# Kernel tuning notes

Measured on AMD Instinct MI355X. Metric: run time of the kernel, lower is better.

Reference implementation:

```python
import jax, jax.numpy as jnp
import numpy as np

N_EXPERTS = 8
TOP_K = 2
W_SCALE = 0.02


def setup_inputs() -> dict:
    key = jax.random.key(0)
    ks = jax.random.split(key, 4)
    S, B, D, F = 2048, 2, 1024, 4096
    x = jax.random.normal(ks[0], (S, B, D), dtype=jnp.float32)
    gate_w = jax.random.normal(ks[1], (D, N_EXPERTS), dtype=jnp.float32) * W_SCALE
    gate_b = jnp.zeros((N_EXPERTS,), dtype=jnp.float32)
    w1 = jax.random.normal(ks[2], (N_EXPERTS, D, F), dtype=jnp.float32) * W_SCALE
    b1 = jnp.zeros((N_EXPERTS, F), dtype=jnp.float32)
    w2 = jax.random.normal(ks[3], (N_EXPERTS, F, D), dtype=jnp.float32) * W_SCALE
    b2 = jnp.zeros((N_EXPERTS, D), dtype=jnp.float32)
    return {"x": x, "gate_w": gate_w, "gate_b": gate_b,
            "w1": w1, "b1": b1, "w2": w2, "b2": b2}


def reference(x, gate_w, gate_b, w1, b1, w2, b2):
    # gate logits: [S, B, E]
    logits = jnp.einsum('sbd,de->sbe', x, gate_w) + gate_b
    top_w, top_idx = jax.lax.top_k(logits, TOP_K)            # [S,B,K]
    # softmax over the top-k logits in float32 (matches dtype=torch.float)
    probs = jax.nn.softmax(top_w.astype(jnp.float32), axis=-1)
    # dense combine weights [S, B, E]: zero for non-selected experts
    comb = jnp.sum(jax.nn.one_hot(top_idx, N_EXPERTS, dtype=probs.dtype)
                   * probs[..., None], axis=-2)
    out = jnp.zeros_like(x)
    for e in range(N_EXPERTS):  # fixed small structural loop over experts
        h = jax.nn.relu(jnp.einsum('sbd,df->sbf', x, w1[e]) + b1[e])
        y = jnp.einsum('sbf,fd->sbd', h, w2[e]) + b2[e]
        out = out + comb[..., e:e + 1].astype(x.dtype) * y
    return out
```

## Files before the change

kernel.cpp:

```cpp
#include <hip/hip_runtime.h>
#include <stdint.h>

#define T_TOK 4096
#define D_DIM 1024
#define F_DIM 4096
#define NEXP 8
#define BM 128
#define BN 128
#define BN2 256
#define BK 32
#define CAP 9216
#define MT_MAX (CAP / BM)

typedef __attribute__((ext_vector_type(8))) short short8;
typedef __attribute__((ext_vector_type(4))) float f4;
typedef __attribute__((ext_vector_type(4))) unsigned short us4;

#define WS_SBASE   64
#define WS_TBASE   96
#define WS_TOPI    256
#define WS_TOPP    (WS_TOPI + T_TOK*2*4)
#define WS_PSLOT   (WS_TOPP + T_TOK*2*4)
#define WS_XG      102400
#define WS_H       (WS_XG + (size_t)CAP*D_DIM*2)
#define WS_Y       (WS_H + (size_t)CAP*F_DIM*2)
#define WS_WT      (WS_Y + (size_t)CAP*D_DIM*2)

__device__ __forceinline__ unsigned short f2bf(float f) {
    union { float f; uint32_t u; } c; c.f = f;
    uint32_t r = c.u + 0x7FFFu + ((c.u >> 16) & 1u);
    return (unsigned short)(r >> 16);
}
__device__ __forceinline__ float bf2f(unsigned short h) {
    union { uint32_t u; float f; } c; c.u = ((uint32_t)h) << 16;
    return c.f;
}

__global__ __launch_bounds__(256) void gate_kernel(
    const float* __restrict__ x, const float* __restrict__ gw,
    const float* __restrict__ gb,
    int* __restrict__ top_idx, float* __restrict__ top_p)
{
    int lane = threadIdx.x & 63;
    int t = blockIdx.x * 4 + (threadIdx.x >> 6);
    const float* xr = x + (size_t)t * D_DIM;
    float acc[8] = {0.f,0.f,0.f,0.f,0.f,0.f,0.f,0.f};
    for (int i = 0; i < 16; ++i) {
        int d = lane + i * 64;
        float xv = xr[d];
        const float* g = gw + d * 8;
        #pragma unroll
        for (int e = 0; e < 8; ++e) acc[e] += xv * g[e];
    }
    #pragma unroll
    for (int e = 0; e < 8; ++e) {
        #pragma unroll
        for (int off = 32; off > 0; off >>= 1)
            acc[e] += __shfl_xor(acc[e], off, 64);
    }
    if (lane == 0) {
        float l[8];
        #pragma unroll
        for (int e = 0; e < 8; ++e) l[e] = acc[e] + gb[e];
        int i0 = 0; float m0 = l[0];
        #pragma unroll
        for (int e = 1; e < 8; ++e) if (l[e] > m0) { m0 = l[e]; i0 = e; }
        int i1 = -1; float m1 = -3.4e38f;
        #pragma unroll
        for (int e = 0; e < 8; ++e) if (e != i0 && l[e] > m1) { m1 = l[e]; i1 = e; }
        float p0 = 1.f / (1.f + expf(m1 - m0));
        top_idx[t*2]   = i0; top_idx[t*2+1] = i1;
        top_p[t*2]     = p0; top_p[t*2+1]   = 1.f - p0;
    }
}

__global__ __launch_bounds__(256) void plan_kernel(
    const int* __restrict__ top_idx, int* __restrict__ sbase,
    int* __restrict__ tbase, int* __restrict__ pslot)
{
    __shared__ int woff[4][8];
    __shared__ int sb_s[8];
    int t = threadIdx.x, wv = t >> 6, lane = t & 63;
    int base = t * 32;

    int h[8] = {0,0,0,0,0,0,0,0};
    for (int i = 0; i < 32; ++i) {
        int e = top_idx[base + i];
        #pragma unroll
        for (int ee = 0; ee < 8; ++ee) h[ee] += (e == ee) ? 1 : 0;
    }
    int inc[8];
    #pragma unroll
    for (int ee = 0; ee < 8; ++ee) {
        int v = h[ee];
        #pragma unroll
        for (int off = 1; off < 64; off <<= 1) {
            int n = __shfl_up(v, off, 64);
            if (lane >= off) v += n;
        }
        inc[ee] = v;
    }
    if (lane == 63) {
        #pragma unroll
        for (int ee = 0; ee < 8; ++ee) woff[wv][ee] = inc[ee];
    }
    __syncthreads();
    if (t == 0) {
        int cnt[8];
        #pragma unroll
        for (int ee = 0; ee < 8; ++ee) {
            int s = 0;
            #pragma unroll
            for (int w = 0; w < 4; ++w) { int v = woff[w][ee]; woff[w][ee] = s; s += v; }
            cnt[ee] = s;
        }
        int b = 0, tb0 = 0;
        tbase[0] = 0;
        #pragma unroll
        for (int e = 0; e < 8; ++e) {
            sb_s[e] = b; sbase[e] = b;
            int mt = (cnt[e] + BM - 1) / BM;
            b += mt * BM; tb0 += mt;
            tbase[e + 1] = tb0;
        }
    }
    __syncthreads();
    int run[8];
    #pragma unroll
    for (int ee = 0; ee < 8; ++ee)
        run[ee] = sb_s[ee] + woff[wv][ee] + inc[ee] - h[ee];
    for (int i = 0; i < 32; ++i) {
        int e = top_idx[base + i];
        int slot = 0;
        #pragma unroll
        for (int ee = 0; ee < 8; ++ee) slot += (e == ee) ? run[ee] : 0;
        pslot[base + i] = slot;
        #pragma unroll
        for (int ee = 0; ee < 8; ++ee) run[ee] += (e == ee) ? 1 : 0;
    }
}

__global__ __launch_bounds__(256) void gather_kernel(
    const float* __restrict__ x, const int* __restrict__ pslot,
    uint16_t* __restrict__ xg)
{
    int t = blockIdx.x;
    int s0 = pslot[2*t], s1 = pslot[2*t + 1];
    int i = threadIdx.x;
    f4 v = ((const f4*)(x + (size_t)t * D_DIM))[i];
    us4 o;
    o.x = f2bf(v[0]); o.y = f2bf(v[1]); o.z = f2bf(v[2]); o.w = f2bf(v[3]);
    *(us4*)(xg + (size_t)s0 * D_DIM + i * 4) = o;
    *(us4*)(xg + (size_t)s1 * D_DIM + i * 4) = o;
}

__global__ __launch_bounds__(512) void convT_kernel(
    const float* __restrict__ W, uint16_t* __restrict__ WT, int K, int N)
{
    __shared__ float ts[64][65];
    int e = blockIdx.z;
    int n0 = blockIdx.x * 64, k0 = blockIdx.y * 64;
    const float* src = W + (size_t)e * K * N + (size_t)k0 * N + n0;
    int t = threadIdx.x;
    int kk = t >> 3, j = t & 7;
    f4 v0 = *(const f4*)(src + (size_t)kk * N + j * 8);
    f4 v1 = *(const f4*)(src + (size_t)kk * N + j * 8 + 4);
    #pragma unroll
    for (int i = 0; i < 4; ++i) ts[j*8 + i][kk] = v0[i];
    #pragma unroll
    for (int i = 0; i < 4; ++i) ts[j*8 + 4 + i][kk] = v1[i];
    __syncthreads();
    int nn = t >> 3;
    short8 o;
    #pragma unroll
    for (int i = 0; i < 8; ++i) o[i] = (short)f2bf(ts[nn][j*8 + i]);
    *(short8*)(WT + (size_t)e * N * K + (size_t)(n0 + nn) * K + k0 + j * 8) = o;
}

template<bool RELU>
__global__ __launch_bounds__(256, 3) void moe_gemm3(
    const uint16_t* __restrict__ A, const uint16_t* __restrict__ Bt,
    const float* __restrict__ bias, uint16_t* __restrict__ Cc,
    const int* __restrict__ tbase, const int* __restrict__ sbase,
    int K, int N, int NT)
{
    __shared__ uint16_t As3[3][BM][BK];
    __shared__ uint16_t Bs3[3][BN][BK];

    int nwg = gridDim.x;
    int lin = blockIdx.x;
    int wg = (lin & 7) * (nwg >> 3) + (lin >> 3);
    int q = wg >> 2;
    int nt = q % NT;
    int mt = (wg & 3) + (q / NT) * 4;

    if (mt >= tbase[8]) return;
    int e = 0;
    while (mt >= tbase[e + 1]) ++e;
    int row0 = sbase[e] + (mt - tbase[e]) * BM;
    int n0 = nt * BN;
    const uint16_t* Be = Bt + (size_t)e * N * K + (size_t)n0 * K;

    int tid = threadIdx.x;
    int wid = tid >> 6, lane = tid & 63;
    int wrow = (wid >> 1) * 64, wcol = (wid & 1) * 64;

    f4 acc[4][4] = {};

    int ovb = tid * 16;
    int rowA[2], koffA[2];
    #pragma unroll
    for (int j = 0; j < 2; ++j) {
        int ov = ovb + j * 4096;
        int row = ov >> 6;
        int cb  = (ov >> 4) & 3;
        rowA[j]  = row;
        koffA[j] = (cb ^ ((row >> 1) & 3)) << 3;
    }

    int abyte[4], bbyte[4];
    #pragma unroll
    for (int m = 0; m < 4; ++m) {
        int r = wrow + m * 16 + (lane & 15);
        abyte[m] = r * 64 + ((((lane >> 4) ^ ((r >> 1) & 3))) << 4);
    }
    #pragma unroll
    for (int n = 0; n < 4; ++n) {
        int c = wcol + n * 16 + (lane & 15);
        bbyte[n] = c * 64 + ((((lane >> 4) ^ ((c >> 1) & 3))) << 4);
    }
    const char* As0 = (const char*)&As3[0][0][0];
    const char* Bs0 = (const char*)&Bs3[0][0][0];

    auto STAGE = [&](int buf, int kt) {
        #pragma unroll
        for (int j = 0; j < 2; ++j) {
            const uint16_t* gpA = A + (size_t)(row0 + rowA[j]) * K + kt + koffA[j];
            __builtin_amdgcn_global_load_lds(
                (const __attribute__((address_space(1))) void*)gpA,
                (__attribute__((address_space(3))) void*)((char*)&As3[buf][0][0] + ovb + j * 4096),
                16, 0, 0);
            const uint16_t* gpB = Be + (size_t)rowA[j] * K + kt + koffA[j];
            __builtin_amdgcn_global_load_lds(
                (const __attribute__((address_space(1))) void*)gpB,
                (__attribute__((address_space(3))) void*)((char*)&Bs3[buf][0][0] + ovb + j * 4096),
                16, 0, 0);
        }
    };

    int nkt = K / BK;
    STAGE(0, 0);
    STAGE(1, BK);
    asm volatile("s_waitcnt vmcnt(4)" ::: "memory");
    __builtin_amdgcn_s_barrier();

    int buf = 0;
    for (int t = 0; t < nkt; ++t) {
        int cb = buf * 8192;
        short8 af[4], bfr[4];
        #pragma unroll
        for (int m = 0; m < 4; ++m) af[m] = *(const short8*)(As0 + cb + abyte[m]);
        #pragma unroll
        for (int n = 0; n < 4; ++n) bfr[n] = *(const short8*)(Bs0 + cb + bbyte[n]);

        bool stg = (t + 2) < nkt;
        if (stg) {
            int b2 = buf + 2; if (b2 >= 3) b2 -= 3;
            STAGE(b2, (t + 2) * BK);
        }

        #pragma unroll
        for (int m = 0; m < 4; ++m)
            #pragma unroll
            for (int n = 0; n < 4; ++n)
                acc[m][n] = __builtin_amdgcn_mfma_f32_16x16x32_bf16(
                    af[m], bfr[n], acc[m][n], 0, 0, 0);

        if (stg) asm volatile("s_waitcnt vmcnt(4)" ::: "memory");
        else     asm volatile("s_waitcnt vmcnt(0)" ::: "memory");
        __builtin_amdgcn_s_barrier();
        buf = (buf + 1 == 3) ? 0 : buf + 1;
    }

    #pragma unroll
    for (int n = 0; n < 4; ++n) {
        int c = wcol + n * 16 + (lane & 15);
        float bv = bias[(size_t)e * N + n0 + c];
        #pragma unroll
        for (int m = 0; m < 4; ++m) {
            int rb = wrow + m * 16 + (lane >> 4) * 4;
            #pragma unroll
            for (int r = 0; r < 4; ++r) {
                float v = acc[m][n][r] + bv;
                if (RELU) v = fmaxf(v, 0.f);
                Cc[(size_t)(row0 + rb + r) * N + n0 + c] = f2bf(v);
            }
        }
    }
}

template<bool RELU>
__global__ __launch_bounds__(512, 4) void moe_gemm6(
    const uint16_t* __restrict__ A, const uint16_t* __restrict__ Bt,
    const float* __restrict__ bias, uint16_t* __restrict__ Cc,
    const int* __restrict__ tbase, const int* __restrict__ sbase,
    int K, int N, int NT)
{
    __shared__ uint16_t As3[3][BM][BK];
    __shared__ uint16_t Bs3[3][BN2][BK];

    int nwg = gridDim.x;
    int lin = blockIdx.x;
    int wg = (lin & 7) * (nwg >> 3) + (lin >> 3);
    int q = wg >> 2;
    int nt = q % NT;
    int mt = (wg & 3) + (q / NT) * 4;

    if (mt >= tbase[8]) return;
    int e = 0;
    while (mt >= tbase[e + 1]) ++e;
    int row0 = sbase[e] + (mt - tbase[e]) * BM;
    int n0 = nt * BN2;
    const uint16_t* Be = Bt + (size_t)e * N * K + (size_t)n0 * K;

    int tid = threadIdx.x;
    int wid = tid >> 6, lane = tid & 63;
    int wrow = (wid >> 2) * 64, wcol = (wid & 3) * 64;
    int lq = lane >> 4, lr = lane & 15;

    f4 acc[4][4] = {};

    int ovb = tid * 16;
    int rowS[2], koffS[2];
    #pragma unroll
    for (int j = 0; j < 2; ++j) {
        int ov = ovb + j * 8192;
        int row = ov >> 6;
        int cb  = (ov >> 4) & 3;
        rowS[j]  = row;
        koffS[j] = (cb ^ ((row >> 1) & 3)) << 3;
    }

    int abyte[4], bbyte[4];
    #pragma unroll
    for (int m = 0; m < 4; ++m) {
        int r = wrow + m * 16 + lr;
        abyte[m] = r * 64 + (((lq ^ ((r >> 1) & 3))) << 4);
    }
    #pragma unroll
    for (int n = 0; n < 4; ++n) {
        int c = wcol + n * 16 + lr;
        bbyte[n] = c * 64 + (((lq ^ ((c >> 1) & 3))) << 4);
    }
    const char* As0 = (const char*)&As3[0][0][0];
    const char* Bs0 = (const char*)&Bs3[0][0][0];

    auto STAGE = [&](int buf, int kt) {
        const uint16_t* gpA = A + (size_t)(row0 + rowS[0]) * K + kt + koffS[0];
        __builtin_amdgcn_global_load_lds(
            (const __attribute__((address_space(1))) void*)gpA,
            (__attribute__((address_space(3))) void*)((char*)&As3[buf][0][0] + ovb),
            16, 0, 0);
        #pragma unroll
        for (int j = 0; j < 2; ++j) {
            const uint16_t* gpB = Be + (size_t)rowS[j] * K + kt + koffS[j];
            __builtin_amdgcn_global_load_lds(
                (const __attribute__((address_space(1))) void*)gpB,
                (__attribute__((address_space(3))) void*)((char*)&Bs3[buf][0][0] + ovb + j * 8192),
                16, 0, 0);
        }
    };

    int nkt = K / BK;
    STAGE(0, 0);
    STAGE(1, BK);
    asm volatile("s_waitcnt vmcnt(3)" ::: "memory");
    __builtin_amdgcn_s_barrier();

    int buf = 0;
    for (int t = 0; t < nkt; ++t) {
        int cba = buf * 8192, cbb = buf * 16384;
        short8 af[4], bfr[4];
        #pragma unroll
        for (int m = 0; m < 4; ++m) af[m] = *(const short8*)(As0 + cba + abyte[m]);
        #pragma unroll
        for (int n = 0; n < 4; ++n) bfr[n] = *(const short8*)(Bs0 + cbb + bbyte[n]);

        bool stg = (t + 2) < nkt;
        if (stg) {
            int b2 = buf + 2; if (b2 >= 3) b2 -= 3;
            STAGE(b2, (t + 2) * BK);
        }

        #pragma unroll
        for (int m = 0; m < 4; ++m)
            #pragma unroll
            for (int n = 0; n < 4; ++n)
                acc[m][n] = __builtin_amdgcn_mfma_f32_16x16x32_bf16(
                    af[m], bfr[n], acc[m][n], 0, 0, 0);

        if (stg) asm volatile("s_waitcnt vmcnt(3)" ::: "memory");
        else     asm volatile("s_waitcnt vmcnt(0)" ::: "memory");
        __builtin_amdgcn_s_barrier();
        buf = (buf + 1 == 3) ? 0 : buf + 1;
    }

    #pragma unroll
    for (int n = 0; n < 4; ++n) {
        int c = wcol + n * 16 + lr;
        float bv = bias[(size_t)e * N + n0 + c];
        #pragma unroll
        for (int m = 0; m < 4; ++m) {
            int rb = wrow + m * 16 + lq * 4;
            #pragma unroll
            for (int r = 0; r < 4; ++r) {
                float v = acc[m][n][r] + bv;
                if (RELU) v = fmaxf(v, 0.f);
                Cc[(size_t)(row0 + rb + r) * N + n0 + c] = f2bf(v);
            }
        }
    }
}

__global__ __launch_bounds__(256) void combine_kernel(
    const uint16_t* __restrict__ Y, const int* __restrict__ pair_slot,
    const float* __restrict__ top_p, float* __restrict__ out)
{
    int t = blockIdx.x;
    int s0 = pair_slot[t*2], s1 = pair_slot[t*2+1];
    float p0 = top_p[t*2],  p1 = top_p[t*2+1];
    int i = threadIdx.x * 4;
    us4 a = *(const us4*)(Y + (size_t)s0 * D_DIM + i);
    us4 b = *(const us4*)(Y + (size_t)s1 * D_DIM + i);
    f4 o;
    o[0] = p0 * bf2f(a.x) + p1 * bf2f(b.x);
    o[1] = p0 * bf2f(a.y) + p1 * bf2f(b.y);
    o[2] = p0 * bf2f(a.z) + p1 * bf2f(b.z);
    o[3] = p0 * bf2f(a.w) + p1 * bf2f(b.w);
    *(f4*)(out + (size_t)t * D_DIM + i) = o;
}

extern "C" void kernel_launch(void* const* d_in, const int* in_sizes, int n_in,
                              void* d_out, int out_size, void* d_ws, size_t ws_size,
                              hipStream_t stream)
{
    const float* x  = (const float*)d_in[0];
    const float* gw = (const float*)d_in[1];
    const float* gb = (const float*)d_in[2];
    const float* w1 = (const float*)d_in[3];
    const float* b1 = (const float*)d_in[4];
    const float* w2 = (const float*)d_in[5];
    const float* b2 = (const float*)d_in[6];
    float* out = (float*)d_out;

    char* ws = (char*)d_ws;
    int*   sbase = (int*)(ws + WS_SBASE);
    int*   tbase = (int*)(ws + WS_TBASE);
    int*   topi  = (int*)(ws + WS_TOPI);
    float* topp  = (float*)(ws + WS_TOPP);
    int*   pslot = (int*)(ws + WS_PSLOT);
    uint16_t* xg = (uint16_t*)(ws + WS_XG);
    uint16_t* H  = (uint16_t*)(ws + WS_H);
    uint16_t* Y  = (uint16_t*)(ws + WS_Y);
    uint16_t* WT = (uint16_t*)(ws + WS_WT);

    gate_kernel<<<T_TOK / 4, 256, 0, stream>>>(x, gw, gb, topi, topp);
    plan_kernel<<<1, 256, 0, stream>>>(topi, sbase, tbase, pslot);
    gather_kernel<<<T_TOK, 256, 0, stream>>>(x, pslot, xg);

    convT_kernel<<<dim3(F_DIM/64, D_DIM/64, NEXP), 512, 0, stream>>>(w1, WT, D_DIM, F_DIM);
    moe_gemm6<true ><<<MT_MAX * (F_DIM / BN2), 512, 0, stream>>>(
        xg, WT, b1, H, tbase, sbase, D_DIM, F_DIM, F_DIM / BN2);
    convT_kernel<<<dim3(D_DIM/64, F_DIM/64, NEXP), 512, 0, stream>>>(w2, WT, F_DIM, D_DIM);
    moe_gemm3<false><<<MT_MAX * (D_DIM / BN), 256, 0, stream>>>(
        H, WT, b2, Y, tbase, sbase, F_DIM, D_DIM, D_DIM / BN);

    combine_kernel<<<T_TOK, 256, 0, stream>>>(Y, pslot, topp, out);
}
```

Measured before the change: 296.4 us.

## Fuse w2 transpose-conversion into first expert GEMM launch to overlap work

Merges the conversion of w2 to transposed bf16 into the same grid as the first expert GEMM, using a separate workspace buffer for the second weight so both can proceed concurrently. The memory-bound conversion blocks can fill idle compute units during the GEMM tail and a kernel launch boundary is removed. The fused kernel reserves the GEMM's large shared allocation even for conversion blocks, which may limit their occupancy, and it needs extra workspace, falling back to the old path otherwise.

```diff
diff --git a/kernel.cpp b/kernel.cpp
--- a/kernel.cpp
+++ b/kernel.cpp
@@ -24,7 +24,10 @@
 #define WS_XG      102400
 #define WS_H       (WS_XG + (size_t)CAP*D_DIM*2)
 #define WS_Y       (WS_H + (size_t)CAP*F_DIM*2)
-#define WS_WT      (WS_Y + (size_t)CAP*D_DIM*2)
+#define WS_WT1     (WS_Y + (size_t)CAP*D_DIM*2)
+#define WT_BYTES   ((size_t)NEXP*D_DIM*F_DIM*2)
+#define WS_WT2     (WS_WT1 + WT_BYTES)
+#define WS_NEED_FUSED (WS_WT2 + WT_BYTES)
 
 __device__ __forceinline__ unsigned short f2bf(float f) {
     union { float f; uint32_t u; } c; c.f = f;
@@ -154,12 +157,12 @@
     *(us4*)(xg + (size_t)s1 * D_DIM + i * 4) = o;
 }
 
-__global__ __launch_bounds__(512) void convT_kernel(
+__device__ __forceinline__ void convT_body(
+    char* smemraw, int nx, int ky, int e,
     const float* __restrict__ W, uint16_t* __restrict__ WT, int K, int N)
 {
-    __shared__ float ts[64][65];
-    int e = blockIdx.z;
-    int n0 = blockIdx.x * 64, k0 = blockIdx.y * 64;
+    float (*ts)[65] = (float(*)[65])smemraw;
+    int n0 = nx * 64, k0 = ky * 64;
     const float* src = W + (size_t)e * K * N + (size_t)k0 * N + n0;
     int t = threadIdx.x;
     int kk = t >> 3, j = t & 7;
@@ -175,6 +178,166 @@
     #pragma unroll
     for (int i = 0; i < 8; ++i) o[i] = (short)f2bf(ts[nn][j*8 + i]);
     *(short8*)(WT + (size_t)e * N * K + (size_t)(n0 + nn) * K + k0 + j * 8) = o;
+}
+
+__global__ __launch_bounds__(512) void convT_kernel(
+    const float* __restrict__ W, uint16_t* __restrict__ WT, int K, int N)
+{
+    __shared__ __align__(16) char smem[16640];
+    convT_body(smem, blockIdx.x, blockIdx.y, blockIdx.z, W, WT, K, N);
+}
+
+template<bool RELU>
+__device__ __forceinline__ void gemm6_body(
+    char* smemraw, int lin, int nwg,
+    const uint16_t* __restrict__ A, const uint16_t* __restrict__ Bt,
+    const float* __restrict__ bias, uint16_t* __restrict__ Cc,
+    const int* __restrict__ tbase, const int* __restrict__ sbase,
+    int K, int N, int NT)
+{
+    char* As0c = smemraw;
+    char* Bs0c = smemraw + 24576;
+
+    int wg = (lin & 7) * (nwg >> 3) + (lin >> 3);
+    int q = wg >> 2;
+    int nt = q % NT;
+    int mt = (wg & 3) + (q / NT) * 4;
+
+    if (mt >= tbase[8]) return;
+    int e = 0;
+    while (mt >= tbase[e + 1]) ++e;
+    int row0 = sbase[e] + (mt - tbase[e]) * BM;
+    int n0 = nt * BN2;
+    const uint16_t* Be = Bt + (size_t)e * N * K + (size_t)n0 * K;
+
+    int tid = threadIdx.x;
+    int wid = tid >> 6, lane = tid & 63;
+    int wrow = (wid >> 2) * 64, wcol = (wid & 3) * 64;
+    int lq = lane >> 4, lr = lane & 15;
+
+    f4 acc[4][4] = {};
+
+    int ovb = tid * 16;
+    int rowS[2], koffS[2];
+    #pragma unroll
+    for (int j = 0; j < 2; ++j) {
+        int ov = ovb + j * 8192;
+        int row = ov >> 6;
+        int cb  = (ov >> 4) & 3;
+        rowS[j]  = row;
+        koffS[j] = (cb ^ ((row >> 1) & 3)) << 3;
+    }
+
+    int abyte[4], bbyte[4];
+    #pragma unroll
+    for (int m = 0; m < 4; ++m) {
+        int r = wrow + m * 16 + lr;
+        abyte[m] = r * 64 + (((lq ^ ((r >> 1) & 3))) << 4);
+    }
+    #pragma unroll
+    for (int n = 0; n < 4; ++n) {
+        int c = wcol + n * 16 + lr;
+        bbyte[n] = c * 64 + (((lq ^ ((c >> 1) & 3))) << 4);
+    }
+
+    auto STAGE = [&](int buf, int kt) {
+        const uint16_t* gpA = A + (size_t)(row0 + rowS[0]) * K + kt + koffS[0];
+        __builtin_amdgcn_global_load_lds(
+            (const __attribute__((address_space(1))) void*)gpA,
+            (__attribute__((address_space(3))) void*)(As0c + buf * 8192 + ovb),
+            16, 0, 0);
+        #pragma unroll
+        for (int j = 0; j < 2; ++j) {
+            const uint16_t* gpB = Be + (size_t)rowS[j] * K + kt + koffS[j];
+            __builtin_amdgcn_global_load_lds(
+                (const __attribute__((address_space(1))) void*)gpB,
+                (__attribute__((address_space(3))) void*)(Bs0c + buf * 16384 + ovb + j * 8192),
+                16, 0, 0);
+        }
+    };
+
+    int nkt = K / BK;
+    STAGE(0, 0);
+    STAGE(1, BK);
+    asm volatile("s_waitcnt vmcnt(3)" ::: "memory");
+    __builtin_amdgcn_s_barrier();
+
+    int buf = 0;
+    for (int t = 0; t < nkt; ++t) {
+        int cba = buf * 8192, cbb = buf * 16384;
+        short8 af[4], bfr[4];
+        #pragma unroll
+        for (int m = 0; m < 4; ++m) af[m] = *(const short8*)(As0c + cba + abyte[m]);
+        #pragma unroll
+        for (int n = 0; n < 4; ++n) bfr[n] = *(const short8*)(Bs0c + cbb + bbyte[n]);
+
+        bool stg = (t + 2) < nkt;
+        if (stg) {
+            int b2 = buf + 2; if (b2 >= 3) b2 -= 3;
+            STAGE(b2, (t + 2) * BK);
+        }
+
+        #pragma unroll
+        for (int m = 0; m < 4; ++m)
+            #pragma unroll
+            for (int n = 0; n < 4; ++n)
+                acc[m][n] = __builtin_amdgcn_mfma_f32_16x16x32_bf16(
+                    af[m], bfr[n], acc[m][n], 0, 0, 0);
+
+        if (stg) asm volatile("s_waitcnt vmcnt(3)" ::: "memory");
+        else     asm volatile("s_waitcnt vmcnt(0)" ::: "memory");
+        __builtin_amdgcn_s_barrier();
+        buf = (buf + 1 == 3) ? 0 : buf + 1;
+    }
+
+    #pragma unroll
+    for (int n = 0; n < 4; ++n) {
+        int c = wcol + n * 16 + lr;
+        float bv = bias[(size_t)e * N + n0 + c];
+        #pragma unroll
+        for (int m = 0; m < 4; ++m) {
+            int rb = wrow + m * 16 + lq * 4;
+            #pragma unroll
+            for (int r = 0; r < 4; ++r) {
+                float v = acc[m][n][r] + bv;
+                if (RELU) v = fmaxf(v, 0.f);
+                Cc[(size_t)(row0 + rb + r) * N + n0 + c] = f2bf(v);
+            }
+        }
+    }
+}
+
+template<bool RELU>
+__global__ __launch_bounds__(512, 4) void moe_gemm6(
+    const uint16_t* __restrict__ A, const uint16_t* __restrict__ Bt,
+    const float* __restrict__ bias, uint16_t* __restrict__ Cc,
+    const int* __restrict__ tbase, const int* __restrict__ sbase,
+    int K, int N, int NT)
+{
+    __shared__ __align__(16) char smem[73728];
+    gemm6_body<RELU>(smem, blockIdx.x, gridDim.x, A, Bt, bias, Cc,
+                     tbase, sbase, K, N, NT);
+}
+
+__global__ __launch_bounds__(512, 4) void gemm1_convw2_fused(
+    const uint16_t* __restrict__ A, const uint16_t* __restrict__ Bt,
+    const float* __restrict__ bias, uint16_t* __restrict__ Cc,
+    const int* __restrict__ tbase, const int* __restrict__ sbase,
+    int K, int N, int NT, int g1,
+    const float* __restrict__ W2, uint16_t* __restrict__ WT2, int K2, int N2)
+{
+    __shared__ __align__(16) char smem[73728];
+    int bid = blockIdx.x;
+    if (bid < g1) {
+        gemm6_body<true>(smem, bid, g1, A, Bt, bias, Cc, tbase, sbase, K, N, NT);
+    } else {
+        int b2 = bid - g1;
+        int e  = b2 >> 10;
+        int rem = b2 & 1023;
+        int ky = rem >> 4;
+        int nx = rem & 15;
+        convT_body(smem, nx, ky, e, W2, WT2, K2, N2);
+    }
 }
 
 template<bool RELU>
@@ -289,129 +452,6 @@
         #pragma unroll
         for (int m = 0; m < 4; ++m) {
             int rb = wrow + m * 16 + (lane >> 4) * 4;
-            #pragma unroll
-            for (int r = 0; r < 4; ++r) {
-                float v = acc[m][n][r] + bv;
-                if (RELU) v = fmaxf(v, 0.f);
-                Cc[(size_t)(row0 + rb + r) * N + n0 + c] = f2bf(v);
-            }
-        }
-    }
-}
-
-template<bool RELU>
-__global__ __launch_bounds__(512, 4) void moe_gemm6(
-    const uint16_t* __restrict__ A, const uint16_t* __restrict__ Bt,
-    const float* __restrict__ bias, uint16_t* __restrict__ Cc,
-    const int* __restrict__ tbase, const int* __restrict__ sbase,
-    int K, int N, int NT)
-{
-    __shared__ uint16_t As3[3][BM][BK];
-    __shared__ uint16_t Bs3[3][BN2][BK];
-
-    int nwg = gridDim.x;
-    int lin = blockIdx.x;
-    int wg = (lin & 7) * (nwg >> 3) + (lin >> 3);
-    int q = wg >> 2;
-    int nt = q % NT;
-    int mt = (wg & 3) + (q / NT) * 4;
-
-    if (mt >= tbase[8]) return;
-    int e = 0;
-    while (mt >= tbase[e + 1]) ++e;
-    int row0 = sbase[e] + (mt - tbase[e]) * BM;
-    int n0 = nt * BN2;
-    const uint16_t* Be = Bt + (size_t)e * N * K + (size_t)n0 * K;
-
-    int tid = threadIdx.x;
-    int wid = tid >> 6, lane = tid & 63;
-    int wrow = (wid >> 2) * 64, wcol = (wid & 3) * 64;
-    int lq = lane >> 4, lr = lane & 15;
-
-    f4 acc[4][4] = {};
-
-    int ovb = tid * 16;
-    int rowS[2], koffS[2];
-    #pragma unroll
-    for (int j = 0; j < 2; ++j) {
-        int ov = ovb + j * 8192;
-        int row = ov >> 6;
-        int cb  = (ov >> 4) & 3;
-        rowS[j]  = row;
-        koffS[j] = (cb ^ ((row >> 1) & 3)) << 3;
-    }
-
-    int abyte[4], bbyte[4];
-    #pragma unroll
-    for (int m = 0; m < 4; ++m) {
-        int r = wrow + m * 16 + lr;
-        abyte[m] = r * 64 + (((lq ^ ((r >> 1) & 3))) << 4);
-    }
-    #pragma unroll
-    for (int n = 0; n < 4; ++n) {
-        int c = wcol + n * 16 + lr;
-        bbyte[n] = c * 64 + (((lq ^ ((c >> 1) & 3))) << 4);
-    }
-    const char* As0 = (const char*)&As3[0][0][0];
-    const char* Bs0 = (const char*)&Bs3[0][0][0];
-
-    auto STAGE = [&](int buf, int kt) {
-        const uint16_t* gpA = A + (size_t)(row0 + rowS[0]) * K + kt + koffS[0];
-        __builtin_amdgcn_global_load_lds(
-            (const __attribute__((address_space(1))) void*)gpA,
-            (__attribute__((address_space(3))) void*)((char*)&As3[buf][0][0] + ovb),
-            16, 0, 0);
-        #pragma unroll
-        for (int j = 0; j < 2; ++j) {
-            const uint16_t* gpB = Be + (size_t)rowS[j] * K + kt + koffS[j];
-            __builtin_amdgcn_global_load_lds(
-                (const __attribute__((address_space(1))) void*)gpB,
-                (__attribute__((address_space(3))) void*)((char*)&Bs3[buf][0][0] + ovb + j * 8192),
-                16, 0, 0);
-        }
-    };
-
-    int nkt = K / BK;
-    STAGE(0, 0);
-    STAGE(1, BK);
-    asm volatile("s_waitcnt vmcnt(3)" ::: "memory");
-    __builtin_amdgcn_s_barrier();
-
-    int buf = 0;
-    for (int t = 0; t < nkt; ++t) {
-        int cba = buf * 8192, cbb = buf * 16384;
-        short8 af[4], bfr[4];
-        #pragma unroll
-        for (int m = 0; m < 4; ++m) af[m] = *(const short8*)(As0 + cba + abyte[m]);
-        #pragma unroll
-        for (int n = 0; n < 4; ++n) bfr[n] = *(const short8*)(Bs0 + cbb + bbyte[n]);
-
-        bool stg = (t + 2) < nkt;
-        if (stg) {
-            int b2 = buf + 2; if (b2 >= 3) b2 -= 3;
-            STAGE(b2, (t + 2) * BK);
-        }
-
-        #pragma unroll
-        for (int m = 0; m < 4; ++m)
-            #pragma unroll
-            for (int n = 0; n < 4; ++n)
-                acc[m][n] = __builtin_amdgcn_mfma_f32_16x16x32_bf16(
-                    af[m], bfr[n], acc[m][n], 0, 0, 0);
-
-        if (stg) asm volatile("s_waitcnt vmcnt(3)" ::: "memory");
-        else     asm volatile("s_waitcnt vmcnt(0)" ::: "memory");
-        __builtin_amdgcn_s_barrier();
-        buf = (buf + 1 == 3) ? 0 : buf + 1;
-    }
-
-    #pragma unroll
-    for (int n = 0; n < 4; ++n) {
-        int c = wcol + n * 16 + lr;
-        float bv = bias[(size_t)e * N + n0 + c];
-        #pragma unroll
-        for (int m = 0; m < 4; ++m) {
-            int rb = wrow + m * 16 + lq * 4;
             #pragma unroll
             for (int r = 0; r < 4; ++r) {
                 float v = acc[m][n][r] + bv;
@@ -459,21 +499,33 @@
     int*   topi  = (int*)(ws + WS_TOPI);
     float* topp  = (float*)(ws + WS_TOPP);
     int*   pslot = (int*)(ws + WS_PSLOT);
-    uint16_t* xg = (uint16_t*)(ws + WS_XG);
-    uint16_t* H  = (uint16_t*)(ws + WS_H);
-    uint16_t* Y  = (uint16_t*)(ws + WS_Y);
-    uint16_t* WT = (uint16_t*)(ws + WS_WT);
+    uint16_t* xg  = (uint16_t*)(ws + WS_XG);
+    uint16_t* H   = (uint16_t*)(ws + WS_H);
+    uint16_t* Y   = (uint16_t*)(ws + WS_Y);
+    uint16_t* WT1 = (uint16_t*)(ws + WS_WT1);
+    uint16_t* WT2 = (uint16_t*)(ws + WS_WT2);
 
     gate_kernel<<<T_TOK / 4, 256, 0, stream>>>(x, gw, gb, topi, topp);
     plan_kernel<<<1, 256, 0, stream>>>(topi, sbase, tbase, pslot);
     gather_kernel<<<T_TOK, 256, 0, stream>>>(x, pslot, xg);
 
-    convT_kernel<<<dim3(F_DIM/64, D_DIM/64, NEXP), 512, 0, stream>>>(w1, WT, D_DIM, F_DIM);
-    moe_gemm6<true ><<<MT_MAX * (F_DIM / BN2), 512, 0, stream>>>(
-        xg, WT, b1, H, tbase, sbase, D_DIM, F_DIM, F_DIM / BN2);
-    convT_kernel<<<dim3(D_DIM/64, F_DIM/64, NEXP), 512, 0, stream>>>(w2, WT, F_DIM, D_DIM);
-    moe_gemm3<false><<<MT_MAX * (D_DIM / BN), 256, 0, stream>>>(
-        H, WT, b2, Y, tbase, sbase, F_DIM, D_DIM, D_DIM / BN);
+    convT_kernel<<<dim3(F_DIM/64, D_DIM/64, NEXP), 512, 0, stream>>>(w1, WT1, D_DIM, F_DIM);
+
+    const int g1 = MT_MAX * (F_DIM / BN2);
+    if (ws_size >= WS_NEED_FUSED) {
+        const int cblk = NEXP * (F_DIM/64) * (D_DIM/64);
+        gemm1_convw2_fused<<<g1 + cblk, 512, 0, stream>>>(
+            xg, WT1, b1, H, tbase, sbase, D_DIM, F_DIM, F_DIM / BN2, g1,
+            w2, WT2, F_DIM, D_DIM);
+        moe_gemm3<false><<<MT_MAX * (D_DIM / BN), 256, 0, stream>>>(
+            H, WT2, b2, Y, tbase, sbase, F_DIM, D_DIM, D_DIM / BN);
+    } else {
+        moe_gemm6<true><<<g1, 512, 0, stream>>>(
+            xg, WT1, b1, H, tbase, sbase, D_DIM, F_DIM, F_DIM / BN2);
+        convT_kernel<<<dim3(D_DIM/64, F_DIM/64, NEXP), 512, 0, stream>>>(w2, WT1, F_DIM, D_DIM);
+        moe_gemm3<false><<<MT_MAX * (D_DIM / BN), 256, 0, stream>>>(
+            H, WT1, b2, Y, tbase, sbase, F_DIM, D_DIM, D_DIM / BN);
+    }
 
     combine_kernel<<<T_TOK, 256, 0, stream>>>(Y, pslot, topp, out);
 }
```

New measurement: 288.3 us. 2.7% less time.
